# Kernel tuning notes

Measured on AMD Instinct MI355X. Metric: run time of the kernel, lower is better.

Reference implementation:

```python
import jax, jax.numpy as jnp
import numpy as np


def setup_inputs() -> dict:
    key = jax.random.key(0)
    ks = jax.random.split(key, 8)
    B, C, S = 32, 64, 64          # batch, per-atom channels, molecule size
    CC = 128                      # x_concat channels; CC + 2*C == OC
    OC = 256                      # conv block channels
    w = lambda k, shp: jax.random.normal(k, shp, dtype=jnp.float32) * 0.05
    return {
        "x": jax.random.normal(ks[0], (B, C, S), dtype=jnp.float32),
        "xc": jax.random.normal(ks[1], (B, CC, S - 1, S), dtype=jnp.float32),
        "W1": w(ks[2], (OC, OC)), "b1": w(ks[3], (OC,)),
        "W2": w(ks[4], (OC, OC)), "b2": w(ks[5], (OC,)),
        "W3": w(ks[6], (OC, OC)), "b3": w(ks[7], (OC,)),
        "batch_size": B,
        "size": S,
    }


def _conv1x1_relu(h, W, b):
    # 1x1 Conv2d == per-position matmul over channels
    return jax.nn.relu(jnp.einsum('bchw,oc->bohw', h, W) + b[None, :, None, None])


def reference(x, xc, W1, b1, W2, b2, W3, b3, batch_size, size):
    # Build pair matrix: for shift d+1, roll[d, i] = (i - (d+1)) % size
    i = jnp.arange(size)
    d = jnp.arange(1, size)
    idx = (i[None, :] - d[:, None]) % size            # [S-1, S]
    rolled = x[:, :, idx]                              # [B, C, S-1, S] gather
    x_rep = jnp.broadcast_to(x[:, :, None, :], rolled.shape)
    # torch.cat((*x_concat, pair_matrix), dim=1): concat channels then [x_rep, rolled]
    pairs_cat = jnp.concatenate([xc, x_rep, rolled], axis=1)  # [B, OC, S-1, S]
    h = _conv1x1_relu(pairs_cat, W1, b1)
    h = _conv1x1_relu(h, W2, b2)
    h = _conv1x1_relu(h, W3, b3)
    return h
```

## Files before the change

### kernel.cpp

```cpp
#include <hip/hip_runtime.h>
#include <stdint.h>


typedef __attribute__((ext_vector_type(8))) __bf16 bf16x8;
typedef __attribute__((ext_vector_type(4))) float f32x4;
typedef __attribute__((ext_vector_type(4))) unsigned short u16x4;
typedef __attribute__((ext_vector_type(8))) unsigned short u16x8;

__device__ __forceinline__ unsigned short f2bf(float f) {
  unsigned int u = __builtin_bit_cast(unsigned int, f);
  u += 0x7FFFu + ((u >> 16) & 1u);
  return (unsigned short)(u >> 16);
}

__device__ __forceinline__ int xaddr(int pos, int c) {
  int slot = (pos << 3) + ((((c & 63) >> 3) ^ pos) & 7);
  return ((c >> 6) << 13) + (slot << 3) + (c & 7);
}

__global__ void wconv_kernel(const float* __restrict__ W1, const float* __restrict__ W2,
                             const float* __restrict__ W3, unsigned short* __restrict__ wb) {
  int i = (blockIdx.x * 256 + threadIdx.x) * 4;
  const float* Ws[3] = {W1, W2, W3};
#pragma unroll
  for (int L = 0; L < 3; ++L) {
    f32x4 a = *(const f32x4*)(Ws[L] + i);
    u16x4 p;
#pragma unroll
    for (int v = 0; v < 4; ++v) p[v] = f2bf(a[v]);
    *(u16x4*)(wb + L * 65536 + i) = p;
  }
}

__global__ __launch_bounds__(512, 2)
void fused_kernel(const float* __restrict__ x, const float* __restrict__ xc,
                  const unsigned short* __restrict__ wb,
                  const float* __restrict__ b1, const float* __restrict__ b2,
                  const float* __restrict__ b3, float* __restrict__ out) {
  __shared__ __align__(16) unsigned char lraw[65536];
  unsigned short* X = (unsigned short*)lraw;
  float* bounce = (float*)lraw;
  unsigned short* stg0 = (unsigned short*)(lraw + 49152);
  unsigned short* stg1 = (unsigned short*)(lraw + 57344);

  const int r = blockIdx.x;
  const int b0 = r / 63;
  const int dd = r % 63;
  const int d = dd + 1;
  const int tid = threadIdx.x;
  const int lane = tid & 63;
  const int g16 = lane >> 4;
  const int l16 = lane & 15;
  const int wv = tid >> 6;

  auto ldrnd = [&](int rd, f32x4 ld[2]) {
    int rr = rd / 3;
    int ck = rd - rr * 3;
    int b = b0 + 16 * rr;
#pragma unroll
    for (int it = 0; it < 2; ++it) {
      int u = it * 512 + tid, cc = u >> 4, i4 = (u & 15) << 2;
      const float* src = (ck < 2)
          ? xc + (((b * 128 + ck * 64 + cc) * 63) + dd) * 64 + i4
          : x + (b * 64 + cc) * 64 + i4;
      ld[it] = *(const f32x4*)src;
    }
  };

  f32x4 ld[2];
  ldrnd(0, ld);
  for (int rd = 0; rd < 6; ++rd) {
    unsigned short* sb = (rd & 1) ? stg1 : stg0;
#pragma unroll
    for (int it = 0; it < 2; ++it) {
      int u = it * 512 + tid, cc = u >> 4, i4 = (u & 15) << 2;
      u16x4 p;
#pragma unroll
      for (int v = 0; v < 4; ++v) p[v] = f2bf(ld[it][v]);
      *(u16x4*)&sb[cc * 64 + i4] = p;
    }
    if (rd < 5) ldrnd(rd + 1, ld);
    __syncthreads();
    {
      int rr = rd / 3;
      int ck = rd - rr * 3;
      int i = tid & 63;
      int c0 = (tid >> 6) << 3;
      u16x8 p;
#pragma unroll
      for (int j = 0; j < 8; ++j) p[j] = sb[(c0 + j) * 64 + i];
      *(u16x8*)&X[xaddr(rr * 64 + i, ck * 64 + c0)] = p;
    }
  }
  __syncthreads();

  for (int layer = 0; layer < 3; ++layer) {
    const unsigned short* wl = wb + layer * 65536;
    const float* bias = (layer == 0) ? b1 : (layer == 1) ? b2 : b3;
    const bool al3 = (layer == 0);

    f32x4 acc[2][8] = {};
    const int ow = wv * 32;

#pragma unroll 2
    for (int kk = 0; kk < 8; ++kk) {
      int kb = kk * 32 + g16 * 8;
      bool a3 = al3 && (kk >= 6);
      int cc = a3 ? (128 + (kb & 63)) : kb;
      bf16x8 afr[2];
#pragma unroll
      for (int mf = 0; mf < 2; ++mf)
        afr[mf] = __builtin_bit_cast(
            bf16x8, *(const u16x8*)(wl + (ow + mf * 16 + l16) * 256 + kb));
      bf16x8 bfr[4];
#pragma unroll
      for (int nf = 0; nf < 4; ++nf) {
        int i = nf * 16 + l16;
        int ie = a3 ? ((i - d) & 63) : i;
        bfr[nf] = __builtin_bit_cast(bf16x8, *(const u16x8*)&X[xaddr(ie, cc)]);
      }
#pragma unroll
      for (int mf = 0; mf < 2; ++mf)
#pragma unroll
        for (int nf = 0; nf < 4; ++nf)
          acc[mf][nf] = __builtin_amdgcn_mfma_f32_16x16x32_bf16(afr[mf], bfr[nf], acc[mf][nf], 0, 0, 0);
#pragma unroll
      for (int nf = 0; nf < 4; ++nf) {
        int i = nf * 16 + l16;
        int ie = 64 + (a3 ? ((i - d) & 63) : i);
        bfr[nf] = __builtin_bit_cast(bf16x8, *(const u16x8*)&X[xaddr(ie, cc)]);
      }
#pragma unroll
      for (int mf = 0; mf < 2; ++mf)
#pragma unroll
        for (int nf = 0; nf < 4; ++nf)
          acc[mf][4 + nf] = __builtin_amdgcn_mfma_f32_16x16x32_bf16(afr[mf], bfr[nf], acc[mf][4 + nf], 0, 0, 0);
    }
    __syncthreads();

    if (layer < 2) {
#pragma unroll
      for (int mf = 0; mf < 2; ++mf) {
        int o0 = ow + mf * 16 + g16 * 4;
        f32x4 bv = *(const f32x4*)(bias + o0);
#pragma unroll
        for (int nf = 0; nf < 8; ++nf) {
          int pos = nf * 16 + l16;
          u16x4 p;
#pragma unroll
          for (int v = 0; v < 4; ++v)
            p[v] = f2bf(fmaxf(acc[mf][nf][v] + bv[v], 0.f));
          *(u16x4*)&X[xaddr(pos, o0)] = p;
        }
      }
      __syncthreads();
    } else {
      bool first = true;
#pragma unroll
      for (int rr = 0; rr < 2; ++rr) {
#pragma unroll
        for (int h = 0; h < 2; ++h) {
          if (!first) __syncthreads();
          first = false;
          if ((wv >> 2) == h) {
#pragma unroll
            for (int mf = 0; mf < 2; ++mf) {
              int olb = (wv & 3) * 32 + mf * 16 + g16 * 4;
              f32x4 bv = *(const f32x4*)(bias + h * 128 + olb);
#pragma unroll
              for (int nq = 0; nq < 4; ++nq) {
                int pos = nq * 16 + l16;
#pragma unroll
                for (int v = 0; v < 4; ++v) {
                  int ol = olb + v;
                  bounce[ol * 64 + (pos ^ ((ol & 7) << 2))] =
                      fmaxf(acc[mf][rr * 4 + nq][v] + bv[v], 0.f);
                }
              }
            }
          }
          __syncthreads();
          int bq = b0 + 16 * rr;
#pragma unroll
          for (int q = 0; q < 4; ++q) {
            int u = q * 512 + tid;
            int oh = u >> 4;
            int pos4 = (u & 15) << 2;
            f32x4 vv = *(const f32x4*)&bounce[oh * 64 + (pos4 ^ ((oh & 7) << 2))];
            int o = h * 128 + oh;
            *(f32x4*)&out[(((bq * 256 + o) * 63) + dd) * 64 + pos4] = vv;
          }
        }
      }
    }
  }
}

extern "C" void kernel_launch(void* const* d_in, const int* in_sizes, int n_in,
                              void* d_out, int out_size, void* d_ws, size_t ws_size,
                              hipStream_t stream) {
  const float* x  = (const float*)d_in[0];
  const float* xc = (const float*)d_in[1];
  const float* W1 = (const float*)d_in[2];
  const float* b1 = (const float*)d_in[3];
  const float* W2 = (const float*)d_in[4];
  const float* b2 = (const float*)d_in[5];
  const float* W3 = (const float*)d_in[6];
  const float* b3 = (const float*)d_in[7];
  float* out = (float*)d_out;
  unsigned short* wb = (unsigned short*)d_ws;

  wconv_kernel<<<64, 256, 0, stream>>>(W1, W2, W3, wb);
  fused_kernel<<<1008, 512, 0, stream>>>(x, xc, wb, b1, b2, b3, out);
}
```

Measured before the change: 108.9 us.

## Load inputs straight into swizzled LDS and write final layer in one pass

The staged, double-buffered fp32→bf16 input transpose is replaced by per-thread scalar loads. Each thread gathers 8 channels for one position and writes one packed vector into the swizzled X tile, which removes the per-round barriers and the staging buffers. The final-layer epilogue now bounces all 256 output channels through the full 64KB LDS at once instead of two 128-channel halves, so fewer barriers are needed and all waves take part in every pass. The cost is scalar 4-byte global loads instead of vector loads, and the software prefetch overlap from the old staging loop is gone.

```diff
diff --git a/kernel.cpp b/kernel.cpp
--- a/kernel.cpp
+++ b/kernel.cpp
@@ -40,8 +40,6 @@
   __shared__ __align__(16) unsigned char lraw[65536];
   unsigned short* X = (unsigned short*)lraw;
   float* bounce = (float*)lraw;
-  unsigned short* stg0 = (unsigned short*)(lraw + 49152);
-  unsigned short* stg1 = (unsigned short*)(lraw + 57344);
 
   const int r = blockIdx.x;
   const int b0 = r / 63;
@@ -53,43 +51,22 @@
   const int l16 = lane & 15;
   const int wv = tid >> 6;
 
-  auto ldrnd = [&](int rd, f32x4 ld[2]) {
-    int rr = rd / 3;
-    int ck = rd - rr * 3;
-    int b = b0 + 16 * rr;
+  {
+    const int p = tid & 63;
+    const int c0 = (tid >> 6) << 3;
 #pragma unroll
-    for (int it = 0; it < 2; ++it) {
-      int u = it * 512 + tid, cc = u >> 4, i4 = (u & 15) << 2;
-      const float* src = (ck < 2)
-          ? xc + (((b * 128 + ck * 64 + cc) * 63) + dd) * 64 + i4
-          : x + (b * 64 + cc) * 64 + i4;
-      ld[it] = *(const f32x4*)src;
-    }
-  };
-
-  f32x4 ld[2];
-  ldrnd(0, ld);
-  for (int rd = 0; rd < 6; ++rd) {
-    unsigned short* sb = (rd & 1) ? stg1 : stg0;
+    for (int cr = 0; cr < 6; ++cr) {
+      const int rr = cr / 3;
+      const int ck = cr - rr * 3;
+      const int b = b0 + 16 * rr;
+      u16x8 v;
 #pragma unroll
-    for (int it = 0; it < 2; ++it) {
-      int u = it * 512 + tid, cc = u >> 4, i4 = (u & 15) << 2;
-      u16x4 p;
-#pragma unroll
-      for (int v = 0; v < 4; ++v) p[v] = f2bf(ld[it][v]);
-      *(u16x4*)&sb[cc * 64 + i4] = p;
-    }
-    if (rd < 5) ldrnd(rd + 1, ld);
-    __syncthreads();
-    {
-      int rr = rd / 3;
-      int ck = rd - rr * 3;
-      int i = tid & 63;
-      int c0 = (tid >> 6) << 3;
-      u16x8 p;
-#pragma unroll
-      for (int j = 0; j < 8; ++j) p[j] = sb[(c0 + j) * 64 + i];
-      *(u16x8*)&X[xaddr(rr * 64 + i, ck * 64 + c0)] = p;
+      for (int j = 0; j < 8; ++j) {
+        float f = (ck < 2) ? xc[(((b * 128 + ck * 64 + c0 + j) * 63) + dd) * 64 + p]
+                           : x[(b * 64 + c0 + j) * 64 + p];
+        v[j] = f2bf(f);
+      }
+      *(u16x8*)&X[xaddr(rr * 64 + p, ck * 64 + c0)] = v;
     }
   }
   __syncthreads();
@@ -155,42 +132,34 @@
       }
       __syncthreads();
     } else {
-      bool first = true;
 #pragma unroll
       for (int rr = 0; rr < 2; ++rr) {
 #pragma unroll
-        for (int h = 0; h < 2; ++h) {
-          if (!first) __syncthreads();
-          first = false;
-          if ((wv >> 2) == h) {
+        for (int mf = 0; mf < 2; ++mf) {
+          int oh0 = ow + mf * 16 + g16 * 4;
+          f32x4 bv = *(const f32x4*)(bias + oh0);
 #pragma unroll
-            for (int mf = 0; mf < 2; ++mf) {
-              int olb = (wv & 3) * 32 + mf * 16 + g16 * 4;
-              f32x4 bv = *(const f32x4*)(bias + h * 128 + olb);
+          for (int nq = 0; nq < 4; ++nq) {
+            int pos = nq * 16 + l16;
 #pragma unroll
-              for (int nq = 0; nq < 4; ++nq) {
-                int pos = nq * 16 + l16;
-#pragma unroll
-                for (int v = 0; v < 4; ++v) {
-                  int ol = olb + v;
-                  bounce[ol * 64 + (pos ^ ((ol & 7) << 2))] =
-                      fmaxf(acc[mf][rr * 4 + nq][v] + bv[v], 0.f);
-                }
-              }
+            for (int v = 0; v < 4; ++v) {
+              int oh = oh0 + v;
+              bounce[oh * 64 + (pos ^ ((oh & 7) << 2))] =
+                  fmaxf(acc[mf][rr * 4 + nq][v] + bv[v], 0.f);
             }
           }
-          __syncthreads();
-          int bq = b0 + 16 * rr;
+        }
+        __syncthreads();
+        int bq = b0 + 16 * rr;
 #pragma unroll
-          for (int q = 0; q < 4; ++q) {
-            int u = q * 512 + tid;
-            int oh = u >> 4;
-            int pos4 = (u & 15) << 2;
-            f32x4 vv = *(const f32x4*)&bounce[oh * 64 + (pos4 ^ ((oh & 7) << 2))];
-            int o = h * 128 + oh;
-            *(f32x4*)&out[(((bq * 256 + o) * 63) + dd) * 64 + pos4] = vv;
-          }
+        for (int q = 0; q < 8; ++q) {
+          int u = q * 512 + tid;
+          int oh = u >> 4;
+          int pos4 = (u & 15) << 2;
+          f32x4 vv = *(const f32x4*)&bounce[oh * 64 + (pos4 ^ ((oh & 7) << 2))];
+          *(f32x4*)&out[(((bq * 256 + oh) * 63) + dd) * 64 + pos4] = vv;
         }
+        if (rr == 0) __syncthreads();
       }
     }
   }
```

New measurement: 106.1 us. 2.5% less time.
